# Kernel optimization log

Hardware: AMD Instinct MI355X
Metric: run time of the kernel (lower is better)

## Reference

```python
import jax, jax.numpy as jnp
import numpy as np

KH = KW = 3
STRIDE = 1
PAD = 1
DIL = 1


def _bilinear_gather(data, py, px):
    # data: [B,C,H,W]; py,px: [B,KK,Ho,Wo] absolute sample coords
    B, C, H, W = data.shape
    y0 = jnp.floor(py)
    x0 = jnp.floor(px)
    wy1 = py - y0  # frac weights
    wx1 = px - x0
    wy0 = 1.0 - wy1
    wx0 = 1.0 - wx1
    flat = data.reshape(B, C, H * W)

    def gather(yi, xi):
        valid = (yi >= 0) & (yi < H) & (xi >= 0) & (xi < W)
        yc = jnp.clip(yi, 0, H - 1).astype(jnp.int32)
        xc = jnp.clip(xi, 0, W - 1).astype(jnp.int32)
        idx = yc * W + xc  # [B,KK,Ho,Wo]
        vals = jax.vmap(lambda im, ix: im[:, ix])(flat, idx)  # [B,C,KK,Ho,Wo]
        return vals * valid[:, None].astype(data.dtype)

    out = (gather(y0, x0) * (wy0 * wx0)[:, None]
           + gather(y0, x0 + 1) * (wy0 * wx1)[:, None]
           + gather(y0 + 1, x0) * (wy1 * wx0)[:, None]
           + gather(y0 + 1, x0 + 1) * (wy1 * wx1)[:, None])
    return out  # [B,C,KK,Ho,Wo]


def setup_inputs() -> dict:
    key = jax.random.key(0)
    k1, k2, k3 = jax.random.split(key, 3)
    data = jax.random.normal(k1, (8, 64, 128, 128), dtype=jnp.float32)
    offset = jax.random.normal(k2, (8, 18, 128, 128), dtype=jnp.float32)
    n = 64 * KH * KW
    stdv = 1.0 / np.sqrt(n)
    weight = jax.random.uniform(k3, (64, 64, KH, KW), dtype=jnp.float32,
                                minval=-stdv, maxval=stdv)
    return {"data": data, "offset": offset, "weight": weight}


def reference(data, offset, weight):
    B, C, H, W = data.shape
    Ho = (H + 2 * PAD - (DIL * (KH - 1) + 1)) // STRIDE + 1
    Wo = (W + 2 * PAD - (DIL * (KW - 1) + 1)) // STRIDE + 1
    KK = KH * KW
    # offset layout (deformable_groups=1): [B, 2*KK, Ho, Wo], interleaved (dy, dx) per kernel pt
    off = offset.reshape(B, KK, 2, Ho, Wo)
    off_y = off[:, :, 0]  # [B,KK,Ho,Wo]
    off_x = off[:, :, 1]
    ki = (jnp.arange(KK) // KW).astype(data.dtype)  # kernel row
    kj = (jnp.arange(KK) % KW).astype(data.dtype)   # kernel col
    base_y = (jnp.arange(Ho, dtype=data.dtype) * STRIDE - PAD)[None, :, None] \
             + (ki * DIL)[:, None, None]            # [KK,Ho,1]
    base_x = (jnp.arange(Wo, dtype=data.dtype) * STRIDE - PAD)[None, None, :] \
             + (kj * DIL)[:, None, None]            # [KK,1,Wo]
    py = off_y + base_y[None]  # [B,KK,Ho,Wo]
    px = off_x + base_x[None]
    sampled = _bilinear_gather(data, py, px)  # [B,C,KK,Ho,Wo]
    O = weight.shape[0]
    out = jnp.einsum('bckhw,ock->bohw', sampled, weight.reshape(O, C, KK))
    return out
```

## Files before the change

kernel.cpp:

```cpp
#include <hip/hip_runtime.h>

#define HH 128
#define WW 128
#define CC 64
#define OO 64
#define KK 9
#define PLANE (HH * WW)

#define BAND 11
#define PXB 72
#define BAND_B (BAND * 128 * PXB)
#define POOL_SLOTS 64
#define POOL_OFF BAND_B
#define POOL_B (POOL_SLOTS * 144)
#define DESC_OFF (POOL_OFF + POOL_B)
#define LDS_TOTAL (DESC_OFF + KK * 256 * 16)

typedef _Float16 half8v __attribute__((ext_vector_type(8)));
typedef _Float16 half2v __attribute__((ext_vector_type(2)));
typedef float floatx4 __attribute__((ext_vector_type(4)));

__device__ __forceinline__ unsigned pkpair(float a, float b) {
    return __builtin_bit_cast(unsigned, __builtin_amdgcn_cvt_pkrtz(a, b));
}
__device__ __forceinline__ half2v h2(unsigned u) {
    return __builtin_bit_cast(half2v, u);
}

__global__ __launch_bounds__(256)
void prep_kernel(const float* __restrict__ in, const float* __restrict__ wsrc,
                 unsigned short* __restrict__ outT, _Float16* __restrict__ wt4) {
    __shared__ unsigned tile[64 * 36];
    int blk = blockIdx.x;
    int t = threadIdx.x;
    if (blk < 2048) {
        int b = blk & 7;
        int rest = blk >> 3;
        int y = rest >> 1;
        int xh = rest & 1;
        int p = t & 63;
        int cg = t >> 6;
        const float* src = in + (size_t)(b * 64) * PLANE + y * WW + xh * 64 + p;
#pragma unroll
        for (int i = 0; i < 8; ++i) {
            int c0 = cg * 16 + 2 * i;
            float v0 = src[(size_t)c0 * PLANE];
            float v1 = src[(size_t)(c0 + 1) * PLANE];
            unsigned lo = __builtin_bit_cast(unsigned short, (_Float16)v0);
            unsigned hi = __builtin_bit_cast(unsigned short, (_Float16)v1);
            tile[p * 36 + (c0 >> 1)] = lo | (hi << 16);
        }
        __syncthreads();
        int p2 = t >> 2;
        int q = t & 3;
        const unsigned* s = &tile[p2 * 36 + q * 8];
        uint4 w0 = *(const uint4*)s;
        uint4 w1 = *(const uint4*)(s + 4);
        int half = q >> 1;
        char* dst = (char*)outT + ((size_t)(b * 2 + half) << 20)
                  + (size_t)(y * 128 + xh * 64 + p2) * 64 + (q & 1) * 32;
        *(uint4*)dst = w0;
        *(uint4*)(dst + 16) = w1;
    } else {
        int idx = (blk - 2048) * 256 + t;
        if (idx < 2 * KK * 4 * 64 * 8) {
            int j = idx & 7;
            int lane = (idx >> 3) & 63;
            int nt = (idx >> 9) & 3;
            int pk = idx >> 11;
            int k = pk % 9;
            int pass = pk / 9;
            int o = nt * 16 + (lane & 15);
            int c = pass * 32 + (lane >> 4) * 8 + j;
            wt4[idx] = (_Float16)wsrc[(o * 64 + c) * 9 + k];
        }
    }
}

__global__ __launch_bounds__(512, 2)
void deform_mfma_kernel(const unsigned short* __restrict__ dataT,
                        const float* __restrict__ offset,
                        const _Float16* __restrict__ wt4,
                        float* __restrict__ out) {
    __shared__ __align__(16) char SB[LDS_TOTAL];
    __shared__ unsigned ovfSrc[POOL_SLOTS];
    __shared__ int ovfCnt;

    const int t = threadIdx.x;
    const int lane = t & 63;
    const int w = t >> 6;
    const int quad = lane >> 4;
    const int l15 = lane & 15;
    const int raw = blockIdx.x;
    const int b = raw & 7;
    const int ho0 = (raw >> 3) * 2;
    const int bs = min(max(ho0 - 4, 0), HH - BAND);

    if (t == 0) ovfCnt = 0;
    __syncthreads();

#pragma unroll
    for (int i = 0; i < 5; ++i) {
        int u = i * 512 + t;
        if (u < KK * 256) {
            int p = u & 255;
            int k = u >> 8;
            int x = p & 127;
            int ho = ho0 + (p >> 7);
            const float* offp = offset + ((size_t)(b * 18) + 2 * k) * PLANE + ho * WW + x;
            float oy = offp[0];
            float ox = offp[PLANE];
            float py = (float)(ho - 1 + k / 3) + oy;
            float pxx = (float)(x - 1 + k % 3) + ox;
            float y0f = floorf(py);
            float x0f = floorf(pxx);
            float fy = py - y0f;
            float fx = pxx - x0f;
            int y0 = (int)y0f, x0 = (int)x0f;
            int y1 = y0 + 1, x1 = x0 + 1;
            float wy0 = (1.f - fy) * ((y0 >= 0 && y0 < HH) ? 1.f : 0.f);
            float wy1 = fy * ((y1 >= 0 && y1 < HH) ? 1.f : 0.f);
            float wx0 = (1.f - fx) * ((x0 >= 0 && x0 < WW) ? 1.f : 0.f);
            float wx1 = fx * ((x1 >= 0 && x1 < WW) ? 1.f : 0.f);
            int yc0 = min(max(y0, 0), HH - 1);
            int yc1 = min(max(y1, 0), HH - 1);
            int x_lo = min(max(x0, 0), WW - 2);
            float wA = ((x0 == x_lo) ? wx0 : 0.f) + ((x1 == x_lo) ? wx1 : 0.f);
            float wB = ((x0 == x_lo + 1) ? wx0 : 0.f) + ((x1 == x_lo + 1) ? wx1 : 0.f);

            unsigned off0, off1;
            {
                int r = yc0 - bs;
                if (wy0 == 0.f) off0 = (unsigned)(x_lo * PXB);
                else if ((unsigned)r < BAND) off0 = (unsigned)((r * 128 + x_lo) * PXB);
                else {
                    int slot = atomicAdd(&ovfCnt, 1);
                    if (slot < POOL_SLOTS) {
                        ovfSrc[slot] = (unsigned)((yc0 * 128 + x_lo) * 64);
                        off0 = (unsigned)(POOL_OFF + slot * 144);
                    } else {
                        int rc = min(max(r, 0), BAND - 1);
                        off0 = (unsigned)((rc * 128 + x_lo) * PXB);
                    }
                }
            }
            {
                int r = yc1 - bs;
                if (wy1 == 0.f) off1 = (unsigned)(x_lo * PXB);
                else if ((unsigned)r < BAND) off1 = (unsigned)((r * 128 + x_lo) * PXB);
                else {
                    int slot = atomicAdd(&ovfCnt, 1);
                    if (slot < POOL_SLOTS) {
                        ovfSrc[slot] = (unsigned)((yc1 * 128 + x_lo) * 64);
                        off1 = (unsigned)(POOL_OFF + slot * 144);
                    } else {
                        int rc = min(max(r, 0), BAND - 1);
                        off1 = (unsigned)((rc * 128 + x_lo) * PXB);
                    }
                }
            }
            uint4 d;
            d.x = (off0 >> 3) | ((off1 >> 3) << 16);
            d.y = pkpair(wy0 * wA, wy0 * wB);
            d.z = pkpair(wy1 * wA, wy1 * wB);
            d.w = 0;
            *(uint4*)(SB + DESC_OFF + (size_t)(k * 256 + p) * 16) = d;
        }
    }
    __syncthreads();
    const int cnt = min(ovfCnt, POOL_SLOTS);

    floatx4 acc[2][4];
#pragma unroll
    for (int mt = 0; mt < 2; ++mt)
#pragma unroll
        for (int nt = 0; nt < 4; ++nt)
            acc[mt][nt] = (floatx4){0.f, 0.f, 0.f, 0.f};

    const unsigned qoff = (unsigned)(quad * 16);

    for (int pass = 0; pass < 2; ++pass) {
        if (pass) __syncthreads();
        const char* gh = (const char*)dataT + ((size_t)(b * 2 + pass) << 20);
        {
            const char* gsrc = gh + (unsigned)(bs * 8192);
#pragma unroll
            for (int i = 0; i < 11; ++i) {
                int u = i * 512 + t;
                uint4 v = *(const uint4*)(gsrc + (size_t)u * 16);
                int pxl = u >> 2, q = u & 3;
                *(uint4*)(SB + pxl * PXB + q * 16) = v;
            }
            if (t < cnt * 8) {
                int s = t >> 3, j = t & 7, ps = j >> 2, q = j & 3;
                uint4 v = *(const uint4*)(gh + ovfSrc[s] + ps * 64 + q * 16);
                *(uint4*)(SB + POOL_OFF + s * 144 + ps * 72 + q * 16) = v;
            }
        }
        __syncthreads();

        for (int k = 0; k < KK; ++k) {
            uint4 bfr[4];
            const uint4* wk = (const uint4*)wt4 + (size_t)((pass * 9 + k) * 4) * 64 + lane;
#pragma unroll
            for (int nt = 0; nt < 4; ++nt) bfr[nt] = wk[nt * 64];

#pragma unroll
            for (int mt = 0; mt < 2; ++mt) {
                int p = w * 32 + mt * 16 + l15;
                uint4 d = *(const uint4*)(SB + DESC_OFF + (size_t)(k * 256 + p) * 16);
                unsigned off0 = (d.x & 0xffffu) << 3;
                unsigned off1 = (d.x >> 16) << 3;
                half2v wv0 = h2(d.y), wv1 = h2(d.z);
                half2v h00 = __builtin_shufflevector(wv0, wv0, 0, 0);
                half2v h01 = __builtin_shufflevector(wv0, wv0, 1, 1);
                half2v h10 = __builtin_shufflevector(wv1, wv1, 0, 0);
                half2v h11 = __builtin_shufflevector(wv1, wv1, 1, 1);
                uint4 v00 = *(const uint4*)(SB + off0 + qoff);
                uint4 v01 = *(const uint4*)(SB + off0 + 72 + qoff);
                uint4 v10 = *(const uint4*)(SB + off1 + qoff);
                uint4 v11 = *(const uint4*)(SB + off1 + 72 + qoff);
                half2v s0 = h2(v00.x) * h00 + h2(v01.x) * h01 + h2(v10.x) * h10 + h2(v11.x) * h11;
                half2v s1 = h2(v00.y) * h00 + h2(v01.y) * h01 + h2(v10.y) * h10 + h2(v11.y) * h11;
                half2v s2 = h2(v00.z) * h00 + h2(v01.z) * h01 + h2(v10.z) * h10 + h2(v11.z) * h11;
                half2v s3 = h2(v00.w) * h00 + h2(v01.w) * h01 + h2(v10.w) * h10 + h2(v11.w) * h11;
                uint4 sv = make_uint4(__builtin_bit_cast(unsigned, s0),
                                      __builtin_bit_cast(unsigned, s1),
                                      __builtin_bit_cast(unsigned, s2),
                                      __builtin_bit_cast(unsigned, s3));
                half8v afrag = __builtin_bit_cast(half8v, sv);
#pragma unroll
                for (int nt = 0; nt < 4; ++nt)
                    acc[mt][nt] = __builtin_amdgcn_mfma_f32_16x16x32_f16(
                        afrag, __builtin_bit_cast(half8v, bfr[nt]), acc[mt][nt], 0, 0, 0);
            }
        }
    }

#pragma unroll
    for (int mt = 0; mt < 2; ++mt)
#pragma unroll
        for (int nt = 0; nt < 4; ++nt) {
            int o = nt * 16 + l15;
            int p = w * 32 + mt * 16 + quad * 4;
            int ho = ho0 + (p >> 7);
            int x = p & 127;
            float* dst = out + (size_t)(b * 64 + o) * PLANE + ho * 128 + x;
            *(floatx4*)dst = acc[mt][nt];
        }
}

__global__ void transpose_weight_kernel(const float* __restrict__ w,
                                        float* __restrict__ wt) {
    int i = blockIdx.x * 256 + threadIdx.x;
    if (i < CC * KK * OO) {
        int o = i & 63;
        int ck = i >> 6;
        wt[i] = w[o * (CC * KK) + ck];
    }
}

__global__ __launch_bounds__(256)
void deform_conv_kernel(const float* __restrict__ data,
                        const float* __restrict__ offset,
                        const float* __restrict__ wt,
                        float* __restrict__ out) {
    const int tid = threadIdx.x;
    const int wo = tid & 127;
    int ohalf = tid >> 7;
    ohalf = __builtin_amdgcn_readfirstlane(ohalf);
    const int row = blockIdx.x;
    const int b = row >> 7;
    const int ho = row & 127;
    int abyte[KK][4];
    float wgt[KK][4];
    const float* offBase = offset + ((size_t)b * 18) * PLANE + ho * WW + wo;
#pragma unroll
    for (int k = 0; k < KK; ++k) {
        float oy = offBase[(2 * k) * PLANE];
        float ox = offBase[(2 * k + 1) * PLANE];
        float py = oy + (float)(ho - 1 + k / 3);
        float px = ox + (float)(wo - 1 + k % 3);
        float y0f = floorf(py);
        float x0f = floorf(px);
        float wy1 = py - y0f, wx1 = px - x0f;
        float wy0 = 1.f - wy1, wx0 = 1.f - wx1;
        int y0 = (int)y0f, x0 = (int)x0f;
        int y1 = y0 + 1, x1 = x0 + 1;
        float my0 = (y0 >= 0 && y0 < HH) ? 1.f : 0.f;
        float my1 = (y1 >= 0 && y1 < HH) ? 1.f : 0.f;
        float mx0 = (x0 >= 0 && x0 < WW) ? 1.f : 0.f;
        float mx1 = (x1 >= 0 && x1 < WW) ? 1.f : 0.f;
        int yc0 = min(max(y0, 0), HH - 1);
        int yc1 = min(max(y1, 0), HH - 1);
        int xc0 = min(max(x0, 0), WW - 1);
        int xc1 = min(max(x1, 0), WW - 1);
        abyte[k][0] = (yc0 * WW + xc0) * 4;
        abyte[k][1] = (yc0 * WW + xc1) * 4;
        abyte[k][2] = (yc1 * WW + xc0) * 4;
        abyte[k][3] = (yc1 * WW + xc1) * 4;
        wgt[k][0] = wy0 * wx0 * my0 * mx0;
        wgt[k][1] = wy0 * wx1 * my0 * mx1;
        wgt[k][2] = wy1 * wx0 * my1 * mx0;
        wgt[k][3] = wy1 * wx1 * my1 * mx1;
    }
    float acc[32];
#pragma unroll
    for (int j = 0; j < 32; ++j) acc[j] = 0.f;
    const float* planeBase = data + (size_t)b * CC * PLANE;
    const float4* wt4base = (const float4*)wt + ohalf * 8;
    for (int c = 0; c < CC; ++c) {
        const char* pc = (const char*)(planeBase + c * PLANE);
#pragma unroll
        for (int k = 0; k < KK; ++k) {
            float v00 = *(const float*)(pc + abyte[k][0]);
            float v01 = *(const float*)(pc + abyte[k][1]);
            float v10 = *(const float*)(pc + abyte[k][2]);
            float v11 = *(const float*)(pc + abyte[k][3]);
            float s = wgt[k][0] * v00 + wgt[k][1] * v01 +
                      wgt[k][2] * v10 + wgt[k][3] * v11;
            const float4* wp = wt4base + (c * KK + k) * 16;
#pragma unroll
            for (int j = 0; j < 8; ++j) {
                float4 wv = wp[j];
                acc[4 * j + 0] += s * wv.x;
                acc[4 * j + 1] += s * wv.y;
                acc[4 * j + 2] += s * wv.z;
                acc[4 * j + 3] += s * wv.w;
            }
        }
    }
    float* outp = out + ((size_t)b * OO + ohalf * 32) * PLANE + ho * WW + wo;
#pragma unroll
    for (int j = 0; j < 32; ++j) outp[j * PLANE] = acc[j];
}

extern "C" void kernel_launch(void* const* d_in, const int* in_sizes, int n_in,
                              void* d_out, int out_size, void* d_ws, size_t ws_size,
                              hipStream_t stream) {
    const float* data = (const float*)d_in[0];
    const float* offset = (const float*)d_in[1];
    const float* weight = (const float*)d_in[2];
    float* out = (float*)d_out;

    const size_t DATA_T_BYTES = (size_t)8 * 2 * 128 * 128 * 64;
    const size_t WT4_BYTES = (size_t)2 * KK * 4 * 64 * 8 * 2;

    if (ws_size >= DATA_T_BYTES + WT4_BYTES) {
        unsigned short* dataT = (unsigned short*)d_ws;
        _Float16* wt4 = (_Float16*)((char*)d_ws + DATA_T_BYTES);
        prep_kernel<<<2048 + 144, 256, 0, stream>>>(data, weight, dataT, wt4);
        deform_mfma_kernel<<<8 * (HH / 2), 512, 0, stream>>>(dataT, offset, wt4, out);
    } else {
        float* wt = (float*)d_ws;
        int nw = CC * KK * OO;
        transpose_weight_kernel<<<(nw + 255) / 256, 256, 0, stream>>>(weight, wt);
        deform_conv_kernel<<<8 * HH, 256, 0, stream>>>(data, offset, wt, out);
    }
}
```

Measured before the change: 130.5 us.

## Use one-row blocks with swizzled LDS band and global fallback for out-of-band taps

Each block now computes a single output row with 256 threads instead of two rows with 512. The LDS band shrinks to 8 rows, stored with an XOR-style quad rotation instead of 72-byte padding, which is meant to avoid bank conflicts. Taps that fall outside the band now read global memory directly, replacing the atomic overflow pool. Per-wave offset and weight descriptors live in compact LDS arrays, and descriptors plus B-fragments for the next tap are prefetched one iteration ahead. The tradeoff is more redundant band loading per output row and divergent global loads for out-of-band samples, in exchange for smaller LDS use, more blocks and simpler setup without an extra barrier.

```diff
diff --git a/kernel.cpp b/kernel.cpp
--- a/kernel.cpp
+++ b/kernel.cpp
@@ -7,14 +7,8 @@
 #define KK 9
 #define PLANE (HH * WW)
 
-#define BAND 11
-#define PXB 72
-#define BAND_B (BAND * 128 * PXB)
-#define POOL_SLOTS 64
-#define POOL_OFF BAND_B
-#define POOL_B (POOL_SLOTS * 144)
-#define DESC_OFF (POOL_OFF + POOL_B)
-#define LDS_TOTAL (DESC_OFF + KK * 256 * 16)
+#define BAND 8
+#define BAND_B (BAND * 128 * 64)
 
 typedef _Float16 half8v __attribute__((ext_vector_type(8)));
 typedef _Float16 half2v __attribute__((ext_vector_type(2)));
@@ -77,14 +71,14 @@
     }
 }
 
-__global__ __launch_bounds__(512, 2)
+__global__ __launch_bounds__(256, 2)
 void deform_mfma_kernel(const unsigned short* __restrict__ dataT,
                         const float* __restrict__ offset,
                         const _Float16* __restrict__ wt4,
                         float* __restrict__ out) {
-    __shared__ __align__(16) char SB[LDS_TOTAL];
-    __shared__ unsigned ovfSrc[POOL_SLOTS];
-    __shared__ int ovfCnt;
+    __shared__ __align__(16) char SB[BAND_B];
+    __shared__ unsigned sOff[KK][128];
+    __shared__ uint2 sWt[KK][128];
 
     const int t = threadIdx.x;
     const int lane = t & 63;
@@ -93,25 +87,21 @@
     const int l15 = lane & 15;
     const int raw = blockIdx.x;
     const int b = raw & 7;
-    const int ho0 = (raw >> 3) * 2;
-    const int bs = min(max(ho0 - 4, 0), HH - BAND);
-
-    if (t == 0) ovfCnt = 0;
-    __syncthreads();
+    const int ho = raw >> 3;
+    const int mbase = w * 32;
+    const int bs = min(max(ho - 3, 0), HH - BAND);
 
 #pragma unroll
     for (int i = 0; i < 5; ++i) {
-        int u = i * 512 + t;
-        if (u < KK * 256) {
-            int p = u & 255;
-            int k = u >> 8;
-            int x = p & 127;
-            int ho = ho0 + (p >> 7);
-            const float* offp = offset + ((size_t)(b * 18) + 2 * k) * PLANE + ho * WW + x;
+        int idx = i * 64 + lane;
+        if (idx < 288) {
+            int k = idx >> 5;
+            int px = mbase + (idx & 31);
+            const float* offp = offset + ((size_t)(b * 18) + 2 * k) * PLANE + ho * WW + px;
             float oy = offp[0];
             float ox = offp[PLANE];
             float py = (float)(ho - 1 + k / 3) + oy;
-            float pxx = (float)(x - 1 + k % 3) + ox;
+            float pxx = (float)(px - 1 + k % 3) + ox;
             float y0f = floorf(py);
             float x0f = floorf(pxx);
             float fy = py - y0f;
@@ -128,47 +118,24 @@
             float wA = ((x0 == x_lo) ? wx0 : 0.f) + ((x1 == x_lo) ? wx1 : 0.f);
             float wB = ((x0 == x_lo + 1) ? wx0 : 0.f) + ((x1 == x_lo + 1) ? wx1 : 0.f);
 
-            unsigned off0, off1;
+            unsigned v0, v1, d;
             {
                 int r = yc0 - bs;
-                if (wy0 == 0.f) off0 = (unsigned)(x_lo * PXB);
-                else if ((unsigned)r < BAND) off0 = (unsigned)((r * 128 + x_lo) * PXB);
-                else {
-                    int slot = atomicAdd(&ovfCnt, 1);
-                    if (slot < POOL_SLOTS) {
-                        ovfSrc[slot] = (unsigned)((yc0 * 128 + x_lo) * 64);
-                        off0 = (unsigned)(POOL_OFF + slot * 144);
-                    } else {
-                        int rc = min(max(r, 0), BAND - 1);
-                        off0 = (unsigned)((rc * 128 + x_lo) * PXB);
-                    }
-                }
+                if (wy0 == 0.f) { v0 = (unsigned)x_lo; d = 0; }
+                else if ((unsigned)r < BAND) { v0 = (unsigned)(r * 128 + x_lo); d = 0; }
+                else { v0 = (unsigned)(yc0 * 128 + x_lo); d = 0x4000u; }
             }
             {
                 int r = yc1 - bs;
-                if (wy1 == 0.f) off1 = (unsigned)(x_lo * PXB);
-                else if ((unsigned)r < BAND) off1 = (unsigned)((r * 128 + x_lo) * PXB);
-                else {
-                    int slot = atomicAdd(&ovfCnt, 1);
-                    if (slot < POOL_SLOTS) {
-                        ovfSrc[slot] = (unsigned)((yc1 * 128 + x_lo) * 64);
-                        off1 = (unsigned)(POOL_OFF + slot * 144);
-                    } else {
-                        int rc = min(max(r, 0), BAND - 1);
-                        off1 = (unsigned)((rc * 128 + x_lo) * PXB);
-                    }
-                }
-            }
-            uint4 d;
-            d.x = (off0 >> 3) | ((off1 >> 3) << 16);
-            d.y = pkpair(wy0 * wA, wy0 * wB);
-            d.z = pkpair(wy1 * wA, wy1 * wB);
-            d.w = 0;
-            *(uint4*)(SB + DESC_OFF + (size_t)(k * 256 + p) * 16) = d;
-        }
-    }
-    __syncthreads();
-    const int cnt = min(ovfCnt, POOL_SLOTS);
+                if (wy1 == 0.f) v1 = (unsigned)x_lo;
+                else if ((unsigned)r < BAND) v1 = (unsigned)(r * 128 + x_lo);
+                else { v1 = (unsigned)(yc1 * 128 + x_lo); d |= 0x20000000u; }
+            }
+            sOff[k][px] = d | v0 | (v1 << 15);
+            sWt[k][px] = make_uint2(pkpair(wy0 * wA, wy0 * wB),
+                                    pkpair(wy1 * wA, wy1 * wB));
+        }
+    }
 
     floatx4 acc[2][4];
 #pragma unroll
@@ -177,7 +144,8 @@
         for (int nt = 0; nt < 4; ++nt)
             acc[mt][nt] = (floatx4){0.f, 0.f, 0.f, 0.f};
 
-    const unsigned qoff = (unsigned)(quad * 16);
+    const int p0 = mbase + l15;
+    const int p1 = mbase + 16 + l15;
 
     for (int pass = 0; pass < 2; ++pass) {
         if (pass) __syncthreads();
@@ -185,41 +153,107 @@
         {
             const char* gsrc = gh + (unsigned)(bs * 8192);
 #pragma unroll
-            for (int i = 0; i < 11; ++i) {
-                int u = i * 512 + t;
+            for (int i = 0; i < 16; ++i) {
+                int u = i * 256 + t;
                 uint4 v = *(const uint4*)(gsrc + (size_t)u * 16);
                 int pxl = u >> 2, q = u & 3;
-                *(uint4*)(SB + pxl * PXB + q * 16) = v;
-            }
-            if (t < cnt * 8) {
-                int s = t >> 3, j = t & 7, ps = j >> 2, q = j & 3;
-                uint4 v = *(const uint4*)(gh + ovfSrc[s] + ps * 64 + q * 16);
-                *(uint4*)(SB + POOL_OFF + s * 144 + ps * 72 + q * 16) = v;
+                *(uint4*)(SB + pxl * 64 + (((q + pxl) & 3) << 4)) = v;
             }
         }
         __syncthreads();
 
+        auto compute = [&](unsigned d, uint2 wp, floatx4* accrow) {
+            unsigned v0 = d & 0x3fffu;
+            unsigned v1 = (d >> 15) & 0x3fffu;
+            unsigned rot00 = ((quad + v0) & 3u) << 4;
+            unsigned rot01 = ((quad + v0 + 1) & 3u) << 4;
+            unsigned rot10 = ((quad + v1) & 3u) << 4;
+            unsigned rot11 = ((quad + v1 + 1) & 3u) << 4;
+            uint4 v00 = *(const uint4*)(SB + ((v0 & 1023u) << 6) + rot00);
+            uint4 v01 = *(const uint4*)(SB + ((v0 & 1023u) << 6) + 64 + rot01);
+            uint4 v10 = *(const uint4*)(SB + ((v1 & 1023u) << 6) + rot10);
+            uint4 v11 = *(const uint4*)(SB + ((v1 & 1023u) << 6) + 64 + rot11);
+            if (d & 0x4000u) {
+                const char* g = gh + ((size_t)v0 << 6) + (quad << 4);
+                v00 = *(const uint4*)g;
+                v01 = *(const uint4*)(g + 64);
+            }
+            if (d & 0x20000000u) {
+                const char* g = gh + ((size_t)v1 << 6) + (quad << 4);
+                v10 = *(const uint4*)g;
+                v11 = *(const uint4*)(g + 64);
+            }
+            half2v wv0 = h2(wp.x), wv1 = h2(wp.y);
+            half2v h00 = __builtin_shufflevector(wv0, wv0, 0, 0);
+            half2v h01 = __builtin_shufflevector(wv0, wv0, 1, 1);
+            half2v h10 = __builtin_shufflevector(wv1, wv1, 0, 0);
+            half2v h11 = __builtin_shufflevector(wv1, wv1, 1, 1);
+            half2v s0 = h2(v00.x) * h00 + h2(v01.x) * h01 + h2(v10.x) * h10 + h2(v11.x) * h11;
+            half2v s1 = h2(v00.y) * h00 + h2(v01.y) * h01 + h2(v10.y) * h10 + h2(v11.y) * h11;
+            half2v s2 = h2(v00.z) * h00 + h2(v01.z) * h01 + h2(v10.z) * h10 + h2(v11.z) * h11;
+            half2v s3 = h2(v00.w) * h00 + h2(v01.w) * h01 + h2(v10.w) * h10 + h2(v11.w) * h11;
+            uint4 sv = make_uint4(__builtin_bit_cast(unsigned, s0),
+                                  __builtin_bit_cast(unsigned, s1),
+                                  __builtin_bit_cast(unsigned, s2),
+                                  __builtin_bit_cast(unsigned, s3));
+            half8v afrag = __builtin_bit_cast(half8v, sv);
+#pragma unroll
+            for (int nt = 0; nt < 4; ++nt)
+                accrow[nt] = __builtin_amdgcn_mfma_f32_16x16x32_f16(
+                    afrag, __builtin_bit_cast(half8v, ((const uint4*)nullptr == nullptr, accrow[nt])), accrow[nt], 0, 0, 0);
+        };
+        (void)compute;
+
+        unsigned dc0 = sOff[0][p0], dc1 = sOff[0][p1];
+        uint2 wc0 = sWt[0][p0], wc1 = sWt[0][p1];
+        uint4 bc[4];
+        {
+            const uint4* wk = (const uint4*)wt4 + (size_t)(pass * 9 * 4) * 64 + lane;
+#pragma unroll
+            for (int nt = 0; nt < 4; ++nt) bc[nt] = wk[nt * 64];
+        }
         for (int k = 0; k < KK; ++k) {
-            uint4 bfr[4];
-            const uint4* wk = (const uint4*)wt4 + (size_t)((pass * 9 + k) * 4) * 64 + lane;
-#pragma unroll
-            for (int nt = 0; nt < 4; ++nt) bfr[nt] = wk[nt * 64];
-
+            unsigned dn0 = 0, dn1 = 0;
+            uint2 wn0 = make_uint2(0, 0), wn1 = make_uint2(0, 0);
+            uint4 bn[4];
+            if (k < 8) {
+                dn0 = sOff[k + 1][p0];
+                dn1 = sOff[k + 1][p1];
+                wn0 = sWt[k + 1][p0];
+                wn1 = sWt[k + 1][p1];
+                const uint4* wk = (const uint4*)wt4 + (size_t)((pass * 9 + k + 1) * 4) * 64 + lane;
+#pragma unroll
+                for (int nt = 0; nt < 4; ++nt) bn[nt] = wk[nt * 64];
+            }
 #pragma unroll
             for (int mt = 0; mt < 2; ++mt) {
-                int p = w * 32 + mt * 16 + l15;
-                uint4 d = *(const uint4*)(SB + DESC_OFF + (size_t)(k * 256 + p) * 16);
-                unsigned off0 = (d.x & 0xffffu) << 3;
-                unsigned off1 = (d.x >> 16) << 3;
-                half2v wv0 = h2(d.y), wv1 = h2(d.z);
+                unsigned d = mt ? dc1 : dc0;
+                uint2 wp = mt ? wc1 : wc0;
+                unsigned v0 = d & 0x3fffu;
+                unsigned v1 = (d >> 15) & 0x3fffu;
+                unsigned rot00 = ((quad + v0) & 3u) << 4;
+                unsigned rot01 = ((quad + v0 + 1) & 3u) << 4;
+                unsigned rot10 = ((quad + v1) & 3u) << 4;
+                unsigned rot11 = ((quad + v1 + 1) & 3u) << 4;
+                uint4 v00 = *(const uint4*)(SB + ((v0 & 1023u) << 6) + rot00);
+                uint4 v01 = *(const uint4*)(SB + ((v0 & 1023u) << 6) + 64 + rot01);
+                uint4 v10 = *(const uint4*)(SB + ((v1 & 1023u) << 6) + rot10);
+                uint4 v11 = *(const uint4*)(SB + ((v1 & 1023u) << 6) + 64 + rot11);
+                if (d & 0x4000u) {
+                    const char* g = gh + ((size_t)v0 << 6) + (quad << 4);
+                    v00 = *(const uint4*)g;
+                    v01 = *(const uint4*)(g + 64);
+                }
+                if (d & 0x20000000u) {
+                    const char* g = gh + ((size_t)v1 << 6) + (quad << 4);
+                    v10 = *(const uint4*)g;
+                    v11 = *(const uint4*)(g + 64);
+                }
+                half2v wv0 = h2(wp.x), wv1 = h2(wp.y);
                 half2v h00 = __builtin_shufflevector(wv0, wv0, 0, 0);
                 half2v h01 = __builtin_shufflevector(wv0, wv0, 1, 1);
                 half2v h10 = __builtin_shufflevector(wv1, wv1, 0, 0);
                 half2v h11 = __builtin_shufflevector(wv1, wv1, 1, 1);
-                uint4 v00 = *(const uint4*)(SB + off0 + qoff);
-                uint4 v01 = *(const uint4*)(SB + off0 + 72 + qoff);
-                uint4 v10 = *(const uint4*)(SB + off1 + qoff);
-                uint4 v11 = *(const uint4*)(SB + off1 + 72 + qoff);
                 half2v s0 = h2(v00.x) * h00 + h2(v01.x) * h01 + h2(v10.x) * h10 + h2(v11.x) * h11;
                 half2v s1 = h2(v00.y) * h00 + h2(v01.y) * h01 + h2(v10.y) * h10 + h2(v11.y) * h11;
                 half2v s2 = h2(v00.z) * h00 + h2(v01.z) * h01 + h2(v10.z) * h10 + h2(v11.z) * h11;
@@ -232,7 +266,12 @@
 #pragma unroll
                 for (int nt = 0; nt < 4; ++nt)
                     acc[mt][nt] = __builtin_amdgcn_mfma_f32_16x16x32_f16(
-                        afrag, __builtin_bit_cast(half8v, bfr[nt]), acc[mt][nt], 0, 0, 0);
+                        afrag, __builtin_bit_cast(half8v, bc[nt]), acc[mt][nt], 0, 0, 0);
+            }
+            if (k < 8) {
+                dc0 = dn0; dc1 = dn1; wc0 = wn0; wc1 = wn1;
+#pragma unroll
+                for (int nt = 0; nt < 4; ++nt) bc[nt] = bn[nt];
             }
         }
     }
@@ -242,10 +281,8 @@
 #pragma unroll
         for (int nt = 0; nt < 4; ++nt) {
             int o = nt * 16 + l15;
-            int p = w * 32 + mt * 16 + quad * 4;
-            int ho = ho0 + (p >> 7);
-            int x = p & 127;
-            float* dst = out + (size_t)(b * 64 + o) * PLANE + ho * 128 + x;
+            int px = mbase + mt * 16 + quad * 4;
+            float* dst = out + (size_t)(b * 64 + o) * PLANE + ho * 128 + px;
             *(floatx4*)dst = acc[mt][nt];
         }
 }
@@ -350,7 +387,7 @@
         unsigned short* dataT = (unsigned short*)d_ws;
         _Float16* wt4 = (_Float16*)((char*)d_ws + DATA_T_BYTES);
         prep_kernel<<<2048 + 144, 256, 0, stream>>>(data, weight, dataT, wt4);
-        deform_mfma_kernel<<<8 * (HH / 2), 512, 0, stream>>>(dataT, offset, wt4, out);
+        deform_mfma_kernel<<<8 * HH, 256, 0, stream>>>(dataT, offset, wt4, out);
     } else {
         float* wt = (float*)d_ws;
         int nw = CC * KK * OO;
```

Measured after the change: 134.8 us. 1.03x slower.
